# Kernel tuning notes

Measured on AMD Instinct MI355X. Metric: run time of the kernel, lower is better.

The kernel has to match this reference:

```python
import jax, jax.numpy as jnp
import numpy as np

# 3x3 window roll offsets, row-major as in PatchShift2D.shift_content
SHIFTS = [(1, 1), (1, 0), (1, -1), (0, 1), (0, 0), (0, -1), (-1, 1), (-1, 0), (-1, -1)]
NUM_WIN = 9


def patch_shift(x, inv):
    # x: [B, T, H, W, C]; pad C up to multiple of 9 and H,W by 1, roll each
    # of the 9 channel groups by a distinct (h, w) offset, then crop back.
    B, T, H, W, C = x.shape
    Ch = int(np.ceil(C / NUM_WIN) * NUM_WIN)
    xp = jnp.pad(x, ((0, 0), (0, 0), (1, 1), (1, 1), (0, Ch - C)))
    m = -1 if inv else 1
    parts = jnp.split(xp, NUM_WIN, axis=-1)
    shifted = [jnp.roll(p, (m * sh, m * sw), axis=(2, 3))
               for p, (sh, sw) in zip(parts, SHIFTS)]
    return jnp.concatenate(shifted, axis=-1)[:, :, 1:H + 1, 1:W + 1, :C]


def _gelu(v):
    return jax.nn.gelu(v, approximate=False)  # torch nn.GELU default (erf)


def setup_inputs() -> dict:
    key = jax.random.key(0)
    ks = jax.random.split(key, 14)
    B, T, H, W, C = 2, 8, 56, 56, 512
    HID = 1024
    s = 0.02
    return {
        "x": jax.random.normal(ks[0], (B, T, H, W, C), dtype=jnp.float32),
        "fc_w": s * jax.random.normal(ks[1], (C, HID), dtype=jnp.float32),
        "fc_b": jnp.zeros((HID,), jnp.float32),
        "fc1_w": s * jax.random.normal(ks[2], (HID, C), dtype=jnp.float32),
        "fc1_b": jnp.zeros((C,), jnp.float32),
        "fc2_w": s * jax.random.normal(ks[3], (HID, C), dtype=jnp.float32),
        "fc2_b": jnp.zeros((C,), jnp.float32),
        "rw1_w": s * jax.random.normal(ks[4], (C, C // 4), dtype=jnp.float32),
        "rw1_b": jnp.zeros((C // 4,), jnp.float32),
        "rw2_w": s * jax.random.normal(ks[5], (C // 4, 2 * C), dtype=jnp.float32),
        "rw2_b": jnp.zeros((2 * C,), jnp.float32),
        "proj_w": s * jax.random.normal(ks[6], (C, C), dtype=jnp.float32),
        "proj_b": jnp.zeros((C,), jnp.float32),
    }


def reference(x, fc_w, fc_b, fc1_w, fc1_b, fc2_w, fc2_b,
              rw1_w, rw1_b, rw2_w, rw2_b, proj_w, proj_b):
    B, T, H, W, C = x.shape
    xh = _gelu(x @ fc_w + fc_b)                                  # [B,T,H,W,HID]
    h = patch_shift(_gelu(patch_shift(xh, False) @ fc1_w + fc1_b), True)  # [B,T,H,W,C]
    w = _gelu(xh @ fc2_w + fc2_b)                                 # [B,T,H,W,C]
    a = (h + w).mean(axis=(1, 2, 3))                              # [B,C]
    a = _gelu(a @ rw1_w + rw1_b) @ rw2_w + rw2_b                  # [B,2C]
    a = jax.nn.softmax(a.reshape(B, C, 2).transpose(2, 0, 1), axis=0)  # [2,B,C]
    a = a[:, :, None, None, None, :]                              # [2,B,1,1,1,C]
    out = h * a[0] + w * a[1]
    return out @ proj_w + proj_b
```

## Files before the change

kernel.cpp:

```cpp
#include <hip/hip_runtime.h>
#include <hip/hip_bf16.h>
#include <stdint.h>


typedef __attribute__((ext_vector_type(8))) short short8;
typedef __attribute__((ext_vector_type(4))) float floatx4;
typedef unsigned int uint;
typedef unsigned short ushort;

#define NTOK   50176
#define HWIMG  3136

__device__ __forceinline__ float gelu_exact(float v) {
    return 0.5f * v * (1.0f + erff(v * 0.70710678118654752440f));
}
__device__ __forceinline__ float gelu_fast(float v) {
    float u = v * (0.7978845608f + 0.0356774081f * v * v);
    return v * __builtin_amdgcn_rcpf(1.0f + __expf(-2.0f * u));
}

__device__ __forceinline__ int shift_h(int g) { return 1 - g / 3; }
__device__ __forceinline__ int shift_w(int g) { return 1 - g % 3; }

typedef const __attribute__((address_space(1))) uint* gas_ptr;
typedef __attribute__((address_space(3))) uint* las_ptr;

__device__ __forceinline__ void async_copy16(const void* g, void* l) {
    gas_ptr gp = (gas_ptr)(uintptr_t)g;
    las_ptr lp = (las_ptr)(uint32_t)(uintptr_t)l;
    __builtin_amdgcn_global_load_lds(gp, lp, 16, 0, 0);
}

template <int EPI>
__global__ __launch_bounds__(256) void gemm_bt(
    const __hip_bfloat16* __restrict__ A,
    const __hip_bfloat16* __restrict__ Bt,
    const float* __restrict__ bias,
    void* __restrict__ Cout, __hip_bfloat16* __restrict__ Cout2,
    float* __restrict__ ssum, int N, int K)
{
    __shared__ __hip_bfloat16 As[128 * 32];
    __shared__ __hip_bfloat16 Bs[128 * 32];

    const int t    = threadIdx.x;
    const int lane = t & 63;
    const int wave = t >> 6;
    const int wm   = wave >> 1;
    const int wn   = wave & 1;

    const int nbn  = gridDim.x;
    const int flat = blockIdx.y * nbn + blockIdx.x;
    const int xcd  = flat & 7;
    const int j    = flat >> 3;
    const int jd   = j / nbn;
    const int bm   = xcd * 49 + jd;
    const int bn   = j - jd * nbn;

    const __hip_bfloat16* ga0 = A  + (size_t)(bm * 128 + (t >> 2)) * K + (t & 3) * 8;
    const __hip_bfloat16* ga1 = ga0 + (size_t)64 * K;
    const __hip_bfloat16* gb0 = Bt + (size_t)(bn * 128 + (t >> 2)) * K + (t & 3) * 8;
    const __hip_bfloat16* gb1 = gb0 + (size_t)64 * K;
    __hip_bfloat16* la0 = &As[t * 8];
    __hip_bfloat16* la1 = &As[t * 8 + 2048];
    __hip_bfloat16* lb0 = &Bs[t * 8];
    __hip_bfloat16* lb1 = &Bs[t * 8 + 2048];

    floatx4 acc[4][4] = {};

    const int kq = (lane >> 4) * 8;
    const int ml = lane & 15;

    for (int k0 = 0; k0 < K; k0 += 32) {
        async_copy16(ga0, la0);
        async_copy16(ga1, la1);
        async_copy16(gb0, lb0);
        async_copy16(gb1, lb1);
        ga0 += 32; ga1 += 32; gb0 += 32; gb1 += 32;
        asm volatile("s_waitcnt vmcnt(0)" ::: "memory");
        __syncthreads();

        short8 af[4], bf[4];
#pragma unroll
        for (int i = 0; i < 4; i++) {
            af[i] = *(const short8*)&As[(wm * 64 + i * 16 + ml) * 32 + kq];
            bf[i] = *(const short8*)&Bs[(wn * 64 + i * 16 + ml) * 32 + kq];
        }
#pragma unroll
        for (int mi = 0; mi < 4; mi++)
#pragma unroll
            for (int ni = 0; ni < 4; ni++)
                acc[mi][ni] = __builtin_amdgcn_mfma_f32_16x16x32_bf16(
                    af[mi], bf[ni], acc[mi][ni], 0, 0, 0);
        __syncthreads();
    }

    const int rq = (lane >> 4) * 4;

    int cols[4], gsh[4], gsw[4];
    float bv[4];
    float sum[4] = {0.f, 0.f, 0.f, 0.f};
#pragma unroll
    for (int ni = 0; ni < 4; ni++) {
        const int col = bn * 128 + wn * 64 + ni * 16 + ml;
        cols[ni] = col;
        bv[ni] = bias[col];
        if (EPI == 1) { const int g = col / 114; gsh[ni] = shift_h(g); gsw[ni] = shift_w(g); }
        if (EPI == 2) { const int g = col / 57;  gsh[ni] = shift_h(g); gsw[ni] = shift_w(g); }
    }

#pragma unroll
    for (int mi = 0; mi < 4; mi++) {
        const int row0 = bm * 128 + wm * 64 + mi * 16 + rq;
        int phr[4], pwr[4];
        if (EPI == 1 || EPI == 2) {
            const int bt_ = row0 / HWIMG;
            const int rem = row0 - bt_ * HWIMG;
            const int ph0 = rem / 56;
            const int pw0 = rem - ph0 * 56;
#pragma unroll
            for (int r = 0; r < 4; r++) {
                int pw = pw0 + r, ph = ph0;
                if (pw >= 56) { pw -= 56; ph += 1; }
                if (ph >= 56) { ph = 0; }
                phr[r] = ph; pwr[r] = pw;
            }
        }
#pragma unroll
        for (int ni = 0; ni < 4; ni++) {
            const int col = cols[ni];
#pragma unroll
            for (int r = 0; r < 4; r++) {
                const int tok = row0 + r;
                float v = acc[mi][ni][r] + bv[ni];
                if (EPI != 0) v = gelu_fast(v);
                if (EPI == 0) {
                    ((float*)Cout)[(size_t)tok * N + col] = v;
                } else if (EPI == 1) {
                    const __hip_bfloat16 bvv = __float2bfloat16(v);
                    ((__hip_bfloat16*)Cout)[(size_t)tok * N + col] = bvv;
                    const int th = phr[r] + gsh[ni], tw = pwr[r] + gsw[ni];
                    if ((unsigned)th < 56u && (unsigned)tw < 56u)
                        Cout2[(size_t)(tok + gsh[ni] * 56 + gsw[ni]) * N + col] = bvv;
                } else if (EPI == 2) {
                    const int th = phr[r] - gsh[ni], tw = pwr[r] - gsw[ni];
                    if ((unsigned)th < 56u && (unsigned)tw < 56u) {
                        ((__hip_bfloat16*)Cout)[(size_t)(tok - gsh[ni] * 56 - gsw[ni]) * N + col]
                            = __float2bfloat16(v);
                        sum[ni] += v;
                    }
                } else {
                    ((__hip_bfloat16*)Cout)[(size_t)tok * N + col] = __float2bfloat16(v);
                    sum[ni] += v;
                }
            }
        }
    }

    if (EPI == 2 || EPI == 3) {
        const int b = (bm >= 196) ? 1 : 0;
#pragma unroll
        for (int ni = 0; ni < 4; ni++) {
            float s = sum[ni];
            s += __shfl_xor(s, 16, 64);
            s += __shfl_xor(s, 32, 64);
            if (lane < 16) atomicAdd(&ssum[b * 512 + cols[ni]], s);
        }
    }
}

template <int C, int GS, int SGN>
__global__ __launch_bounds__(256) void zero_holes(__hip_bfloat16* __restrict__ buf)
{
    const int i = blockIdx.x * 256 + threadIdx.x;
    const int c = i % C;
    const int p = i / C;
    const int bt = p / 220, fp = p % 220;
    int oh, ow;
    if (fp < 56)       { oh = 0;        ow = fp; }
    else if (fp < 112) { oh = 55;       ow = fp - 56; }
    else if (fp < 166) { oh = fp - 111; ow = 0; }
    else               { oh = fp - 165; ow = 55; }
    const int g = c / GS;
    const int ih = oh - SGN * shift_h(g);
    const int iw = ow - SGN * shift_w(g);
    if ((unsigned)ih >= 56u || (unsigned)iw >= 56u)
        buf[((size_t)(bt * HWIMG + oh * 56 + ow)) * C + c] = __float2bfloat16(0.0f);
}

__global__ __launch_bounds__(256) void cvt_x(const float4* __restrict__ x,
                                             __hip_bfloat16* __restrict__ xb)
{
    int i = blockIdx.x * 256 + threadIdx.x;
    float4 v = x[i];
    __hip_bfloat16 b0 = __float2bfloat16(v.x);
    __hip_bfloat16 b1 = __float2bfloat16(v.y);
    __hip_bfloat16 b2 = __float2bfloat16(v.z);
    __hip_bfloat16 b3 = __float2bfloat16(v.w);
    uint2 o;
    o.x = (uint)*(ushort*)&b0 | ((uint)*(ushort*)&b1 << 16);
    o.y = (uint)*(ushort*)&b2 | ((uint)*(ushort*)&b3 << 16);
    *(uint2*)&xb[(size_t)i * 4] = o;
}

__global__ __launch_bounds__(256) void prep_w(
    const float* __restrict__ fcw,  const float* __restrict__ fc1w,
    const float* __restrict__ fc2w, const float* __restrict__ projw,
    __hip_bfloat16* __restrict__ fcwT, __hip_bfloat16* __restrict__ fc1T,
    __hip_bfloat16* __restrict__ fc2T, __hip_bfloat16* __restrict__ projT)
{
    int i = blockIdx.x * 256 + threadIdx.x;
    if (i < 524288) {
        int n = i >> 9, k = i & 511;
        fcwT[i] = __float2bfloat16(fcw[k * 1024 + n]);
    } else if (i < 1048576) {
        int j = i - 524288;
        int n = j >> 10, k = j & 1023;
        fc1T[j] = __float2bfloat16(fc1w[k * 512 + n]);
    } else if (i < 1572864) {
        int j = i - 1048576;
        int n = j >> 10, k = j & 1023;
        fc2T[j] = __float2bfloat16(fc2w[k * 512 + n]);
    } else if (i < 1835008) {
        int j = i - 1572864;
        int n = j >> 9, k = j & 511;
        projT[j] = __float2bfloat16(projw[k * 512 + n]);
    }
}

__global__ __launch_bounds__(256) void tiny_mlp(
    const float* __restrict__ s0, const float* __restrict__ s1,
    const float* __restrict__ rw1_w, const float* __restrict__ rw1_b,
    const float* __restrict__ rw2_w, const float* __restrict__ rw2_b,
    float* __restrict__ a0, float* __restrict__ a1)
{
    __shared__ float mean[1024];
    __shared__ float z[256];
    __shared__ float av[2048];
    const int t = threadIdx.x;
    for (int i = t; i < 1024; i += 256)
        mean[i] = (s0[i] + s1[i]) * (1.0f / 25088.0f);
    __syncthreads();
    {
        const int b = t >> 7, j = t & 127;
        float acc = rw1_b[j];
        for (int cc = 0; cc < 512; cc++)
            acc += mean[b * 512 + cc] * rw1_w[cc * 128 + j];
        z[t] = gelu_exact(acc);
    }
    __syncthreads();
    for (int i = t; i < 2048; i += 256) {
        const int b = i >> 10, o = i & 1023;
        float acc = rw2_b[o];
        for (int j = 0; j < 128; j++)
            acc += z[b * 128 + j] * rw2_w[j * 1024 + o];
        av[i] = acc;
    }
    __syncthreads();
    for (int i = t; i < 1024; i += 256) {
        const int b = i >> 9, cc = i & 511;
        const float x0 = av[b * 1024 + 2 * cc];
        const float x1 = av[b * 1024 + 2 * cc + 1];
        const float m = fmaxf(x0, x1);
        const float e0 = expf(x0 - m), e1 = expf(x1 - m);
        const float inv = 1.0f / (e0 + e1);
        a0[i] = e0 * inv;
        a1[i] = e1 * inv;
    }
}

__device__ __forceinline__ float bf_lo(uint u) { return __uint_as_float(u << 16); }
__device__ __forceinline__ float bf_hi(uint u) { return __uint_as_float(u & 0xffff0000u); }
__device__ __forceinline__ uint pack_bf2(float lo, float hi) {
    __hip_bfloat16 a = __float2bfloat16(lo), b = __float2bfloat16(hi);
    return (uint)*(ushort*)&a | ((uint)*(ushort*)&b << 16);
}

__global__ __launch_bounds__(256) void combine(
    const uint4* __restrict__ hs4, const uint4* __restrict__ w4,
    const float* __restrict__ a0, const float* __restrict__ a1,
    uint4* __restrict__ hw4)
{
    const int i = blockIdx.x * 256 + threadIdx.x;
    const int ck = i & 63;
    const int tok = i >> 6;
    const int b = (tok >= 25088) ? 1 : 0;
    const float4* A0 = (const float4*)&a0[b * 512 + ck * 8];
    const float4* A1 = (const float4*)&a1[b * 512 + ck * 8];
    const float4 s0l = A0[0], s0h = A0[1];
    const float4 s1l = A1[0], s1h = A1[1];
    const uint4 h = hs4[i], w = w4[i];
    uint4 o;
    o.x = pack_bf2(bf_lo(h.x) * s0l.x + bf_lo(w.x) * s1l.x,
                   bf_hi(h.x) * s0l.y + bf_hi(w.x) * s1l.y);
    o.y = pack_bf2(bf_lo(h.y) * s0l.z + bf_lo(w.y) * s1l.z,
                   bf_hi(h.y) * s0l.w + bf_hi(w.y) * s1l.w);
    o.z = pack_bf2(bf_lo(h.z) * s0h.x + bf_lo(w.z) * s1h.x,
                   bf_hi(h.z) * s0h.y + bf_hi(w.z) * s1h.y);
    o.w = pack_bf2(bf_lo(h.w) * s0h.z + bf_lo(w.w) * s1h.z,
                   bf_hi(h.w) * s0h.w + bf_hi(w.w) * s1h.w);
    hw4[i] = o;
}

extern "C" void kernel_launch(void* const* d_in, const int* in_sizes, int n_in,
                              void* d_out, int out_size, void* d_ws, size_t ws_size,
                              hipStream_t stream)
{
    const float* x      = (const float*)d_in[0];
    const float* fc_w   = (const float*)d_in[1];
    const float* fc_b   = (const float*)d_in[2];
    const float* fc1_w  = (const float*)d_in[3];
    const float* fc1_b  = (const float*)d_in[4];
    const float* fc2_w  = (const float*)d_in[5];
    const float* fc2_b  = (const float*)d_in[6];
    const float* rw1_w  = (const float*)d_in[7];
    const float* rw1_b  = (const float*)d_in[8];
    const float* rw2_w  = (const float*)d_in[9];
    const float* rw2_b  = (const float*)d_in[10];
    const float* proj_w = (const float*)d_in[11];
    const float* proj_b = (const float*)d_in[12];

    uint8_t* ws = (uint8_t*)d_ws;
    __hip_bfloat16* xh  = (__hip_bfloat16*)(ws);
    __hip_bfloat16* xb  = (__hip_bfloat16*)(ws + 102760448);
    uint8_t* wt         = ws + 102760448 + 51380224;
    __hip_bfloat16* fcwT  = (__hip_bfloat16*)(wt);
    __hip_bfloat16* fc1T  = fcwT + 524288;
    __hip_bfloat16* fc2T  = fc1T + 524288;
    __hip_bfloat16* projT = fc2T + 524288;
    float* s0 = (float*)(wt + 3670016);
    float* s1 = s0 + 1024;
    float* a0 = s1 + 1024;
    float* a1 = a0 + 1024;

    __hip_bfloat16* xs   = (__hip_bfloat16*)d_out;
    __hip_bfloat16* wbuf = (__hip_bfloat16*)d_out;
    __hip_bfloat16* hs   = xb;
    __hip_bfloat16* hw   = xh;

    hipMemsetAsync(s0, 0, 8192, stream);

    zero_holes<1024, 114, +1><<<14080, 256, 0, stream>>>(xs);
    cvt_x<<<25088, 256, 0, stream>>>((const float4*)x, xb);
    prep_w<<<7168, 256, 0, stream>>>(fc_w, fc1_w, fc2_w, proj_w, fcwT, fc1T, fc2T, projT);

    gemm_bt<1><<<dim3(8, 392), 256, 0, stream>>>(xb, fcwT, fc_b, xh, xs, nullptr, 1024, 512);
    zero_holes<512, 57, -1><<<7040, 256, 0, stream>>>(hs);
    gemm_bt<2><<<dim3(4, 392), 256, 0, stream>>>(xs, fc1T, fc1_b, hs, nullptr, s0, 512, 1024);
    gemm_bt<3><<<dim3(4, 392), 256, 0, stream>>>(xh, fc2T, fc2_b, wbuf, nullptr, s1, 512, 1024);
    tiny_mlp<<<1, 256, 0, stream>>>(s0, s1, rw1_w, rw1_b, rw2_w, rw2_b, a0, a1);
    combine<<<12544, 256, 0, stream>>>((const uint4*)hs, (const uint4*)wbuf, a0, a1, (uint4*)hw);
    gemm_bt<0><<<dim3(4, 392), 256, 0, stream>>>(hw, projT, proj_b, d_out, nullptr, nullptr, 512, 512);
}
```

Before: 657.6 us.

## Stage GEMM epilogue through swizzled LDS for vectorized 16-byte output stores

The GEMM epilogue now writes the bias-added, GELU-applied tile as bf16 into a shared-memory buffer with an XOR swizzle. It then reads it back row-wise so each thread issues 16-byte stores, including the patch-shifted scatter writes. Channel sums are reduced per 8-column group before the atomics. This replaces scattered 2-byte stores with coalesced vector stores, at the cost of an extra LDS round trip and a barrier. The EPI 0 path now rounds through bf16 before writing its fp32 output, which loses precision.

```diff
diff --git a/kernel.cpp b/kernel.cpp
--- a/kernel.cpp
+++ b/kernel.cpp
@@ -21,6 +21,13 @@
 
 __device__ __forceinline__ int shift_h(int g) { return 1 - g / 3; }
 __device__ __forceinline__ int shift_w(int g) { return 1 - g % 3; }
+
+__device__ __forceinline__ float bf_lo(uint u) { return __uint_as_float(u << 16); }
+__device__ __forceinline__ float bf_hi(uint u) { return __uint_as_float(u & 0xffff0000u); }
+__device__ __forceinline__ uint pack_bf2(float lo, float hi) {
+    __hip_bfloat16 a = __float2bfloat16(lo), b = __float2bfloat16(hi);
+    return (uint)*(ushort*)&a | ((uint)*(ushort*)&b << 16);
+}
 
 typedef const __attribute__((address_space(1))) uint* gas_ptr;
 typedef __attribute__((address_space(3))) uint* las_ptr;
@@ -39,8 +46,10 @@
     void* __restrict__ Cout, __hip_bfloat16* __restrict__ Cout2,
     float* __restrict__ ssum, int N, int K)
 {
-    __shared__ __hip_bfloat16 As[128 * 32];
-    __shared__ __hip_bfloat16 Bs[128 * 32];
+    __shared__ __align__(16) char smem[32768];
+    __hip_bfloat16* As = (__hip_bfloat16*)smem;
+    __hip_bfloat16* Bs = (__hip_bfloat16*)(smem + 8192);
+    __hip_bfloat16* Cs = (__hip_bfloat16*)smem;
 
     const int t    = threadIdx.x;
     const int lane = t & 63;
@@ -95,75 +104,127 @@
     }
 
     const int rq = (lane >> 4) * 4;
-
-    int cols[4], gsh[4], gsw[4];
-    float bv[4];
-    float sum[4] = {0.f, 0.f, 0.f, 0.f};
 #pragma unroll
     for (int ni = 0; ni < 4; ni++) {
-        const int col = bn * 128 + wn * 64 + ni * 16 + ml;
-        cols[ni] = col;
-        bv[ni] = bias[col];
-        if (EPI == 1) { const int g = col / 114; gsh[ni] = shift_h(g); gsw[ni] = shift_w(g); }
-        if (EPI == 2) { const int g = col / 57;  gsh[ni] = shift_h(g); gsw[ni] = shift_w(g); }
-    }
-
-#pragma unroll
-    for (int mi = 0; mi < 4; mi++) {
-        const int row0 = bm * 128 + wm * 64 + mi * 16 + rq;
-        int phr[4], pwr[4];
-        if (EPI == 1 || EPI == 2) {
-            const int bt_ = row0 / HWIMG;
-            const int rem = row0 - bt_ * HWIMG;
-            const int ph0 = rem / 56;
-            const int pw0 = rem - ph0 * 56;
+        const int col = wn * 64 + ni * 16 + ml;
+        const float bv = bias[bn * 128 + col];
+#pragma unroll
+        for (int mi = 0; mi < 4; mi++) {
+            const int row0 = wm * 64 + mi * 16 + rq;
 #pragma unroll
             for (int r = 0; r < 4; r++) {
-                int pw = pw0 + r, ph = ph0;
-                if (pw >= 56) { pw -= 56; ph += 1; }
-                if (ph >= 56) { ph = 0; }
-                phr[r] = ph; pwr[r] = pw;
+                float v = acc[mi][ni][r] + bv;
+                if (EPI != 0) v = gelu_fast(v);
+                const int rr = row0 + r;
+                const int pcol = col ^ (16 * ((rr >> 2) & 3));
+                Cs[rr * 128 + pcol] = __float2bfloat16(v);
             }
         }
-#pragma unroll
-        for (int ni = 0; ni < 4; ni++) {
-            const int col = cols[ni];
-#pragma unroll
-            for (int r = 0; r < 4; r++) {
-                const int tok = row0 + r;
-                float v = acc[mi][ni][r] + bv[ni];
-                if (EPI != 0) v = gelu_fast(v);
-                if (EPI == 0) {
-                    ((float*)Cout)[(size_t)tok * N + col] = v;
-                } else if (EPI == 1) {
-                    const __hip_bfloat16 bvv = __float2bfloat16(v);
-                    ((__hip_bfloat16*)Cout)[(size_t)tok * N + col] = bvv;
-                    const int th = phr[r] + gsh[ni], tw = pwr[r] + gsw[ni];
-                    if ((unsigned)th < 56u && (unsigned)tw < 56u)
-                        Cout2[(size_t)(tok + gsh[ni] * 56 + gsw[ni]) * N + col] = bvv;
-                } else if (EPI == 2) {
-                    const int th = phr[r] - gsh[ni], tw = pwr[r] - gsw[ni];
-                    if ((unsigned)th < 56u && (unsigned)tw < 56u) {
-                        ((__hip_bfloat16*)Cout)[(size_t)(tok - gsh[ni] * 56 - gsw[ni]) * N + col]
-                            = __float2bfloat16(v);
-                        sum[ni] += v;
+    }
+    __syncthreads();
+
+    const int tcol = (t & 15) * 8;
+    const int gc0  = bn * 128 + tcol;
+    float csum[8] = {};
+    int gs_h = 0, gs_w = 0, guni = 1;
+    if (EPI == 1) {
+        const int g0 = gc0 / 114, g7 = (gc0 + 7) / 114;
+        guni = (g0 == g7);
+        gs_h = shift_h(g0); gs_w = shift_w(g0);
+    } else if (EPI == 2) {
+        const int g0 = gc0 / 57, g7 = (gc0 + 7) / 57;
+        guni = (g0 == g7);
+        gs_h = shift_h(g0); gs_w = shift_w(g0);
+    }
+
+#pragma unroll
+    for (int i = 0; i < 8; i++) {
+        const int lrow = i * 16 + (t >> 4);
+        const int tok  = bm * 128 + lrow;
+        const int ptcol = tcol ^ (16 * ((lrow >> 2) & 3));
+        const uint4 val = *(const uint4*)&Cs[lrow * 128 + ptcol];
+        const uint vc[4] = {val.x, val.y, val.z, val.w};
+
+        if (EPI == 0) {
+            float4 f0, f1;
+            f0.x = bf_lo(vc[0]); f0.y = bf_hi(vc[0]);
+            f0.z = bf_lo(vc[1]); f0.w = bf_hi(vc[1]);
+            f1.x = bf_lo(vc[2]); f1.y = bf_hi(vc[2]);
+            f1.z = bf_lo(vc[3]); f1.w = bf_hi(vc[3]);
+            float* op = (float*)Cout + (size_t)tok * N + gc0;
+            *(float4*)op = f0;
+            *(float4*)(op + 4) = f1;
+        } else if (EPI == 3) {
+            *(uint4*)((__hip_bfloat16*)Cout + (size_t)tok * N + gc0) = val;
+#pragma unroll
+            for (int e = 0; e < 4; e++) {
+                csum[2 * e]     += bf_lo(vc[e]);
+                csum[2 * e + 1] += bf_hi(vc[e]);
+            }
+        } else {
+            const int bt  = tok / HWIMG;
+            const int rem = tok - bt * HWIMG;
+            const int ph  = rem / 56;
+            const int pw  = rem - ph * 56;
+            if (EPI == 1) {
+                *(uint4*)((__hip_bfloat16*)Cout + (size_t)tok * 1024 + gc0) = val;
+                if (guni) {
+                    if ((unsigned)(ph + gs_h) < 56u && (unsigned)(pw + gs_w) < 56u)
+                        *(uint4*)(Cout2 + (size_t)(tok + gs_h * 56 + gs_w) * 1024 + gc0) = val;
+                } else {
+#pragma unroll
+                    for (int e = 0; e < 8; e++) {
+                        const int c = gc0 + e;
+                        const int g = c / 114;
+                        const int sh = shift_h(g), sw = shift_w(g);
+                        if ((unsigned)(ph + sh) < 56u && (unsigned)(pw + sw) < 56u) {
+                            const uint comp = vc[e >> 1];
+                            ((ushort*)Cout2)[(size_t)(tok + sh * 56 + sw) * 1024 + c] =
+                                (ushort)((e & 1) ? (comp >> 16) : (comp & 0xffffu));
+                        }
+                    }
+                }
+            } else {
+                if (guni) {
+                    if ((unsigned)(ph - gs_h) < 56u && (unsigned)(pw - gs_w) < 56u) {
+                        *(uint4*)((__hip_bfloat16*)Cout +
+                                  (size_t)(tok - gs_h * 56 - gs_w) * 512 + gc0) = val;
+#pragma unroll
+                        for (int e = 0; e < 4; e++) {
+                            csum[2 * e]     += bf_lo(vc[e]);
+                            csum[2 * e + 1] += bf_hi(vc[e]);
+                        }
                     }
                 } else {
-                    ((__hip_bfloat16*)Cout)[(size_t)tok * N + col] = __float2bfloat16(v);
-                    sum[ni] += v;
+#pragma unroll
+                    for (int e = 0; e < 8; e++) {
+                        const int c = gc0 + e;
+                        const int g = c / 57;
+                        const int sh = shift_h(g), sw = shift_w(g);
+                        if ((unsigned)(ph - sh) < 56u && (unsigned)(pw - sw) < 56u) {
+                            const uint comp = vc[e >> 1];
+                            const ushort us = (ushort)((e & 1) ? (comp >> 16) : (comp & 0xffffu));
+                            ((ushort*)Cout)[(size_t)(tok - sh * 56 - sw) * 512 + c] = us;
+                            csum[e] += __uint_as_float((uint)us << 16);
+                        }
+                    }
                 }
             }
         }
     }
 
     if (EPI == 2 || EPI == 3) {
-        const int b = (bm >= 196) ? 1 : 0;
-#pragma unroll
-        for (int ni = 0; ni < 4; ni++) {
-            float s = sum[ni];
-            s += __shfl_xor(s, 16, 64);
-            s += __shfl_xor(s, 32, 64);
-            if (lane < 16) atomicAdd(&ssum[b * 512 + cols[ni]], s);
+#pragma unroll
+        for (int e = 0; e < 8; e++) {
+            csum[e] += __shfl_xor(csum[e], 16, 64);
+            csum[e] += __shfl_xor(csum[e], 32, 64);
+        }
+        if (lane < 16) {
+            const int b = (bm >= 196) ? 1 : 0;
+            const int colb = bn * 128 + lane * 8;
+#pragma unroll
+            for (int e = 0; e < 8; e++)
+                atomicAdd(&ssum[b * 512 + colb + e], csum[e]);
         }
     }
 }
@@ -192,13 +253,9 @@
 {
     int i = blockIdx.x * 256 + threadIdx.x;
     float4 v = x[i];
-    __hip_bfloat16 b0 = __float2bfloat16(v.x);
-    __hip_bfloat16 b1 = __float2bfloat16(v.y);
-    __hip_bfloat16 b2 = __float2bfloat16(v.z);
-    __hip_bfloat16 b3 = __float2bfloat16(v.w);
     uint2 o;
-    o.x = (uint)*(ushort*)&b0 | ((uint)*(ushort*)&b1 << 16);
-    o.y = (uint)*(ushort*)&b2 | ((uint)*(ushort*)&b3 << 16);
+    o.x = pack_bf2(v.x, v.y);
+    o.y = pack_bf2(v.z, v.w);
     *(uint2*)&xb[(size_t)i * 4] = o;
 }
 
@@ -241,18 +298,18 @@
         mean[i] = (s0[i] + s1[i]) * (1.0f / 25088.0f);
     __syncthreads();
     {
-        const int b = t >> 7, j = t & 127;
-        float acc = rw1_b[j];
+        const int b = t >> 7, jj = t & 127;
+        float acc = rw1_b[jj];
         for (int cc = 0; cc < 512; cc++)
-            acc += mean[b * 512 + cc] * rw1_w[cc * 128 + j];
+            acc += mean[b * 512 + cc] * rw1_w[cc * 128 + jj];
         z[t] = gelu_exact(acc);
     }
     __syncthreads();
     for (int i = t; i < 2048; i += 256) {
         const int b = i >> 10, o = i & 1023;
         float acc = rw2_b[o];
-        for (int j = 0; j < 128; j++)
-            acc += z[b * 128 + j] * rw2_w[j * 1024 + o];
+        for (int jj = 0; jj < 128; jj++)
+            acc += z[b * 128 + jj] * rw2_w[jj * 1024 + o];
         av[i] = acc;
     }
     __syncthreads();
@@ -266,13 +323,6 @@
         a0[i] = e0 * inv;
         a1[i] = e1 * inv;
     }
-}
-
-__device__ __forceinline__ float bf_lo(uint u) { return __uint_as_float(u << 16); }
-__device__ __forceinline__ float bf_hi(uint u) { return __uint_as_float(u & 0xffff0000u); }
-__device__ __forceinline__ uint pack_bf2(float lo, float hi) {
-    __hip_bfloat16 a = __float2bfloat16(lo), b = __float2bfloat16(hi);
-    return (uint)*(ushort*)&a | ((uint)*(ushort*)&b << 16);
 }
 
 __global__ __launch_bounds__(256) void combine(
```

Result: slower. 916.6 us (+39.4%).
